# Kernel tuning notes

Hardware: AMD Instinct MI355X
Metric: run time of the kernel (lower is better)

## Reference

```python
import jax, jax.numpy as jnp
import numpy as np

NU = 200000  # num_users
NI = 200000  # num_items
D = 128      # d_model
B = 4096     # interaction batch


def setup_inputs() -> dict:
    key = jax.random.key(0)
    ks = jax.random.split(key, 24)
    f = lambda k, s, sc=1.0: (jax.random.normal(k, s, dtype=jnp.float32) * sc)
    s = 1.0 / np.sqrt(D)
    return {
        "user_id": jax.random.randint(ks[0], (B,), 0, NU),
        "prev_item_id": jax.random.randint(ks[1], (B,), 0, NI),
        "item_id": jax.random.randint(ks[2], (B,), 0, NI),
        "time_since_prev_item": jax.random.uniform(ks[3], (B, 1), dtype=jnp.float32),
        "time_since_prev_user": jax.random.uniform(ks[4], (B, 1), dtype=jnp.float32),
        "dynamic_user_emb": f(ks[5], (NU, D), 0.1),
        "dynamic_item_emb": f(ks[6], (NI, D), 0.1),
        "is_user_new": jnp.ones((NU, 1), dtype=jnp.float32),
        "is_item_new": jnp.ones((NI, 1), dtype=jnp.float32),
        "static_user_W": f(ks[7], (NU, D)),
        "static_item_W": f(ks[8], (NI, D)),
        "initial_user_emb": f(ks[9], (1, D)),
        "initial_item_emb": f(ks[10], (1, D)),
        "user_Wih": f(ks[11], (D, D + 1), s),
        "user_Whh": f(ks[12], (D, D), s),
        "user_bih": f(ks[13], (D,), s),
        "user_bhh": f(ks[14], (D,), s),
        "item_Wih": f(ks[15], (D, D + 1), s),
        "item_Whh": f(ks[16], (D, D), s),
        "item_bih": f(ks[17], (D,), s),
        "item_bhh": f(ks[18], (D,), s),
        "pred_W": f(ks[19], (2 * D, 4 * D), 1.0 / np.sqrt(4 * D)),
        "pred_b": f(ks[20], (2 * D,), 1.0 / np.sqrt(4 * D)),
        "td_W": f(ks[21], (D, 1)),
        "td_b": f(ks[22], (D,)),
    }


def _rnn_cell(x, h, Wih, Whh, bih, bhh):
    # torch.nn.RNNCell: tanh(x @ Wih^T + bih + h @ Whh^T + bhh)
    return jnp.tanh(x @ Wih.T + bih + h @ Whh.T + bhh)


def reference(user_id, prev_item_id, item_id, time_since_prev_item, time_since_prev_user,
              dynamic_user_emb, dynamic_item_emb, is_user_new, is_item_new,
              static_user_W, static_item_W, initial_user_emb, initial_item_emb,
              user_Wih, user_Whh, user_bih, user_bhh,
              item_Wih, item_Whh, item_bih, item_bhh,
              pred_W, pred_b, td_W, td_b):
    # gather dynamic embeddings (fall back to initial emb for new entities)
    user_emb = is_user_new[user_id] * initial_user_emb + dynamic_user_emb[user_id]
    item_emb = is_item_new[item_id] * initial_item_emb + dynamic_item_emb[item_id]
    prev_item_emb = is_item_new[prev_item_id] * initial_item_emb + dynamic_item_emb[prev_item_id]
    static_user_emb = static_user_W[user_id]
    static_item_emb = static_item_W[item_id]
    prev_static_item_emb = static_item_W[prev_item_id]

    # time projection + prediction head
    user_proj = user_emb * (1.0 + time_since_prev_item @ td_W.T + td_b)
    item_pred = jnp.concatenate(
        [user_proj, prev_item_emb, prev_static_item_emb, static_user_emb], axis=1) @ pred_W.T + pred_b
    item_target = jnp.concatenate([item_emb, static_item_emb], axis=1)

    # RNNCell updates
    updated_user_emb = _rnn_cell(jnp.concatenate([item_emb, time_since_prev_item], axis=1),
                                 user_emb, user_Wih, user_Whh, user_bih, user_bhh)
    updated_item_emb = _rnn_cell(jnp.concatenate([user_emb, time_since_prev_user], axis=1),
                                 item_emb, item_Wih, item_Whh, item_bih, item_bhh)

    # scatter back into persistent buffers (detached, as in torch)
    new_dyn_user = dynamic_user_emb.at[user_id].set(jax.lax.stop_gradient(updated_user_emb))
    new_dyn_item = dynamic_item_emb.at[item_id].set(jax.lax.stop_gradient(updated_item_emb))
    new_is_user_new = is_user_new.at[user_id].set(0.0)
    new_is_item_new = is_item_new.at[item_id].set(0.0)

    return (item_pred, item_target, updated_user_emb, user_emb, updated_item_emb, item_emb,
            new_dyn_user, new_dyn_item, new_is_user_new, new_is_item_new)
```

## Files before the change

### kernel.cpp

```cpp
#include <hip/hip_runtime.h>
#include <hip/hip_bf16.h>

#define NU 200000
#define NI 200000
#define D 128
#define BATCH 4096

typedef __bf16 bf16x8 __attribute__((ext_vector_type(8)));
typedef float f32x4 __attribute__((ext_vector_type(4)));

__device__ __forceinline__ void store_bf16x4(__hip_bfloat16* p, float4 v) {
    union { __hip_bfloat16 h[4]; uint2 u; } pk;
    pk.h[0] = __float2bfloat16(v.x);
    pk.h[1] = __float2bfloat16(v.y);
    pk.h[2] = __float2bfloat16(v.z);
    pk.h[3] = __float2bfloat16(v.w);
    *reinterpret_cast<uint2*>(p) = pk.u;
}

__device__ __forceinline__ float4 f4_fma(float s, float4 a, float4 b) {
    return make_float4(fmaf(s, a.x, b.x), fmaf(s, a.y, b.y),
                       fmaf(s, a.z, b.z), fmaf(s, a.w, b.w));
}

__global__ __launch_bounds__(256) void prep_kernel(
    const float* __restrict__ predW,
    const float* __restrict__ uWih, const float* __restrict__ uWhh,
    const float* __restrict__ iWih, const float* __restrict__ iWhh,
    const float* __restrict__ ubih, const float* __restrict__ ubhh,
    const float* __restrict__ ibih, const float* __restrict__ ibhh,
    const int* __restrict__ uid, const int* __restrict__ iid,
    __hip_bfloat16* __restrict__ wPred,
    __hip_bfloat16* __restrict__ wU, __hip_bfloat16* __restrict__ wI,
    float* __restrict__ biasU, float* __restrict__ biasI,
    int* __restrict__ lastU, int* __restrict__ lastI)
{
    int idx = blockIdx.x * 256 + threadIdx.x;
    if (idx < 131072) {
        wPred[idx] = __float2bfloat16(predW[idx]);
        return;
    }
    idx -= 131072;
    if (idx < 73728) {
        int z = idx / 36864;
        int r = idx - z * 36864;
        int j = r / 288, k = r - (r / 288) * 288;
        const float* Wih = z ? iWih : uWih;
        const float* Whh = z ? iWhh : uWhh;
        float v = 0.0f;
        if (k < 128)      v = Whh[j * 128 + k];
        else if (k < 257) v = Wih[j * 129 + (k - 128)];
        __hip_bfloat16* W = z ? wI : wU;
        W[j * 288 + k] = __float2bfloat16(v);
        return;
    }
    idx -= 73728;
    if (idx < 128) { biasU[idx] = ubih[idx] + ubhh[idx]; return; }
    idx -= 128;
    if (idx < 128) { biasI[idx] = ibih[idx] + ibhh[idx]; return; }
    idx -= 128;
    if (idx < BATCH) { atomicMax(&lastU[uid[idx]], idx); return; }
    idx -= BATCH;
    if (idx < BATCH) { atomicMax(&lastI[iid[idx]], idx); return; }
}

__global__ __launch_bounds__(256) void gather_copy_kernel(
    const int* __restrict__ uid, const int* __restrict__ pid,
    const int* __restrict__ iid,
    const float* __restrict__ t_i, const float* __restrict__ t_u,
    const float* __restrict__ dynU, const float* __restrict__ dynI,
    const float* __restrict__ isU, const float* __restrict__ isI,
    const float* __restrict__ statU, const float* __restrict__ statI,
    const float* __restrict__ initU, const float* __restrict__ initI,
    const float* __restrict__ tdW, const float* __restrict__ tdb,
    float* __restrict__ o_user_emb, float* __restrict__ o_item_emb,
    float* __restrict__ o_target,
    __hip_bfloat16* __restrict__ xpred,
    __hip_bfloat16* __restrict__ xhU, __hip_bfloat16* __restrict__ xhI,
    float4* __restrict__ oDynU, float4* __restrict__ oDynI,
    float4* __restrict__ oIsU, float4* __restrict__ oIsI)
{
    long long idx = (long long)blockIdx.x * 256 + threadIdx.x;
    if (idx < 131072) {
        int b = (int)(idx >> 5);
        int g = (int)(idx & 31);
        const float4* dU4 = (const float4*)dynU;
        const float4* dI4 = (const float4*)dynI;
        const float4* sU4 = (const float4*)statU;
        const float4* sI4 = (const float4*)statI;

        int u = uid[b], i = iid[b], p = pid[b];
        float fu = isU[u], fi = isI[i], fp = isI[p];
        float ti = t_i[b], tu = t_u[b];

        float4 iu = ((const float4*)initU)[g];
        float4 ii = ((const float4*)initI)[g];
        float4 ue = f4_fma(fu, iu, dU4[(size_t)u * 32 + g]);
        float4 ie = f4_fma(fi, ii, dI4[(size_t)i * 32 + g]);
        float4 pe = f4_fma(fp, ii, dI4[(size_t)p * 32 + g]);
        float4 su = sU4[(size_t)u * 32 + g];
        float4 si = sI4[(size_t)i * 32 + g];
        float4 sp = sI4[(size_t)p * 32 + g];
        float4 tw = ((const float4*)tdW)[g];
        float4 tb = ((const float4*)tdb)[g];

        ((float4*)o_user_emb)[(size_t)b * 32 + g] = ue;
        ((float4*)o_item_emb)[(size_t)b * 32 + g] = ie;
        ((float4*)o_target)[(size_t)b * 64 + g] = ie;
        ((float4*)o_target)[(size_t)b * 64 + 32 + g] = si;

        float4 f = f4_fma(ti, tw, tb);
        float4 proj = make_float4(ue.x * (1.0f + f.x), ue.y * (1.0f + f.y),
                                  ue.z * (1.0f + f.z), ue.w * (1.0f + f.w));

        __hip_bfloat16* xp = xpred + (size_t)b * 512;
        store_bf16x4(xp + 4 * g, proj);
        store_bf16x4(xp + 128 + 4 * g, pe);
        store_bf16x4(xp + 256 + 4 * g, sp);
        store_bf16x4(xp + 384 + 4 * g, su);

        __hip_bfloat16* xu = xhU + (size_t)b * 288;
        store_bf16x4(xu + 4 * g, ue);
        store_bf16x4(xu + 128 + 4 * g, ie);
        __hip_bfloat16* xi = xhI + (size_t)b * 288;
        store_bf16x4(xi + 4 * g, ie);
        store_bf16x4(xi + 128 + 4 * g, ue);
        if (g < 8) {
            float4 zu = make_float4(g == 0 ? ti : 0.0f, 0.0f, 0.0f, 0.0f);
            float4 zi = make_float4(g == 0 ? tu : 0.0f, 0.0f, 0.0f, 0.0f);
            store_bf16x4(xu + 256 + 4 * g, zu);
            store_bf16x4(xi + 256 + 4 * g, zi);
        }
        return;
    }
    idx -= 131072;
    if (idx < 6400000) { oDynU[idx] = ((const float4*)dynU)[idx]; return; }
    idx -= 6400000;
    if (idx < 6400000) { oDynI[idx] = ((const float4*)dynI)[idx]; return; }
    idx -= 6400000;
    if (idx < 50000) { oIsU[idx] = ((const float4*)isU)[idx]; return; }
    idx -= 50000;
    if (idx < 50000) { oIsI[idx] = ((const float4*)isI)[idx]; return; }
}

__global__ __launch_bounds__(256) void gemm_fused(
    const __hip_bfloat16* __restrict__ xpred,
    const __hip_bfloat16* __restrict__ wPred,
    const float* __restrict__ predb, float* __restrict__ o_pred,
    const __hip_bfloat16* __restrict__ xhU, const __hip_bfloat16* __restrict__ xhI,
    const __hip_bfloat16* __restrict__ wU, const __hip_bfloat16* __restrict__ wI,
    const float* __restrict__ biasU, const float* __restrict__ biasI,
    const int* __restrict__ uid, const int* __restrict__ iid,
    const int* __restrict__ lastU, const int* __restrict__ lastI,
    float* __restrict__ o_updU, float* __restrict__ o_updI,
    float* __restrict__ o_dynU, float* __restrict__ o_dynI,
    float* __restrict__ o_isU, float* __restrict__ o_isI)
{
    int bx = blockIdx.x;
    int tid = threadIdx.x;
    int wave = tid >> 6, lane = tid & 63, quad = lane >> 4, l15 = lane & 15;

    if (bx < 256) {
        const int K = 512;
        int m0 = (bx & 63) * 64, n0 = (bx >> 6) * 64;
        f32x4 acc[4] = {};
        const __hip_bfloat16* Arow = xpred + (size_t)(m0 + wave * 16 + l15) * K;
        for (int k0 = 0; k0 < K; k0 += 32) {
            bf16x8 a = *reinterpret_cast<const bf16x8*>(Arow + k0 + quad * 8);
#pragma unroll
            for (int ct = 0; ct < 4; ++ct) {
                bf16x8 b = *reinterpret_cast<const bf16x8*>(
                    wPred + (size_t)(n0 + ct * 16 + l15) * K + k0 + quad * 8);
                acc[ct] = __builtin_amdgcn_mfma_f32_16x16x32_bf16(a, b, acc[ct], 0, 0, 0);
            }
        }
        int orow = m0 + wave * 16 + quad * 4;
#pragma unroll
        for (int ct = 0; ct < 4; ++ct) {
            int col = n0 + ct * 16 + l15;
            float bc = predb[col];
#pragma unroll
            for (int r = 0; r < 4; ++r)
                o_pred[(size_t)(orow + r) * 256 + col] = acc[ct][r] + bc;
        }
    } else {
        bx -= 256;
        int z = bx >> 7; bx &= 127;
        int m0 = (bx & 63) * 64, n0 = (bx >> 6) * 64;
        const __hip_bfloat16* A = z ? xhI : xhU;
        const __hip_bfloat16* W = z ? wI : wU;
        const float* bias = z ? biasI : biasU;
        const int* ids  = z ? iid : uid;
        const int* last = z ? lastI : lastU;
        float* outB = z ? o_updI : o_updU;
        float* outD = z ? o_dynI : o_dynU;
        float* oIs  = z ? o_isI  : o_isU;

        const int K = 288;
        f32x4 acc[4] = {};
        const __hip_bfloat16* Arow = A + (size_t)(m0 + wave * 16 + l15) * K;
        for (int k0 = 0; k0 < K; k0 += 32) {
            bf16x8 a = *reinterpret_cast<const bf16x8*>(Arow + k0 + quad * 8);
#pragma unroll
            for (int ct = 0; ct < 4; ++ct) {
                bf16x8 b = *reinterpret_cast<const bf16x8*>(
                    W + (size_t)(n0 + ct * 16 + l15) * K + k0 + quad * 8);
                acc[ct] = __builtin_amdgcn_mfma_f32_16x16x32_bf16(a, b, acc[ct], 0, 0, 0);
            }
        }
        int orow = m0 + wave * 16 + quad * 4;
        int rid[4], win[4];
#pragma unroll
        for (int r = 0; r < 4; ++r) {
            int row = orow + r;
            rid[r] = ids[row];
            win[r] = (last[rid[r]] == row);
        }
#pragma unroll
        for (int ct = 0; ct < 4; ++ct) {
            int col = n0 + ct * 16 + l15;
            float bc = bias[col];
#pragma unroll
            for (int r = 0; r < 4; ++r) {
                float v = tanhf(acc[ct][r] + bc);
                outB[(size_t)(orow + r) * D + col] = v;
                if (win[r]) outD[(size_t)rid[r] * D + col] = v;
            }
        }
        if (n0 == 0 && l15 == 0) {
#pragma unroll
            for (int r = 0; r < 4; ++r) oIs[rid[r]] = 0.0f;
        }
    }
}

extern "C" void kernel_launch(void* const* d_in, const int* in_sizes, int n_in,
                              void* d_out, int out_size, void* d_ws, size_t ws_size,
                              hipStream_t stream) {
    const int*   uid   = (const int*)d_in[0];
    const int*   pid   = (const int*)d_in[1];
    const int*   iid   = (const int*)d_in[2];
    const float* t_i   = (const float*)d_in[3];
    const float* t_u   = (const float*)d_in[4];
    const float* dynU  = (const float*)d_in[5];
    const float* dynI  = (const float*)d_in[6];
    const float* isU   = (const float*)d_in[7];
    const float* isI   = (const float*)d_in[8];
    const float* statU = (const float*)d_in[9];
    const float* statI = (const float*)d_in[10];
    const float* initU = (const float*)d_in[11];
    const float* initI = (const float*)d_in[12];
    const float* uWih  = (const float*)d_in[13];
    const float* uWhh  = (const float*)d_in[14];
    const float* ubih  = (const float*)d_in[15];
    const float* ubhh  = (const float*)d_in[16];
    const float* iWih  = (const float*)d_in[17];
    const float* iWhh  = (const float*)d_in[18];
    const float* ibih  = (const float*)d_in[19];
    const float* ibhh  = (const float*)d_in[20];
    const float* predW = (const float*)d_in[21];
    const float* predb = (const float*)d_in[22];
    const float* tdW   = (const float*)d_in[23];
    const float* tdb   = (const float*)d_in[24];

    float* out = (float*)d_out;
    float* o_pred     = out;
    float* o_target   = out + 1048576;
    float* o_updU     = out + 2097152;
    float* o_userEmb  = out + 2621440;
    float* o_updI     = out + 3145728;
    float* o_itemEmb  = out + 3670016;
    float* o_dynU     = out + 4194304;
    float* o_dynI     = out + 29794304;
    float* o_isU      = out + 55394304;
    float* o_isI      = out + 55594304;

    char* ws = (char*)d_ws;
    int* lastU = (int*)ws;
    int* lastI = lastU + NU;
    __hip_bfloat16* xpred = (__hip_bfloat16*)(ws + 1600000);
    __hip_bfloat16* xhU   = (__hip_bfloat16*)(ws + 5794304);
    __hip_bfloat16* xhI   = (__hip_bfloat16*)(ws + 8153600);
    __hip_bfloat16* wPred = (__hip_bfloat16*)(ws + 10512896);
    __hip_bfloat16* wU    = (__hip_bfloat16*)(ws + 10775040);
    __hip_bfloat16* wI    = (__hip_bfloat16*)(ws + 10848768);
    float* biasU = (float*)(ws + 10922496);
    float* biasI = (float*)(ws + 10923008);

    hipMemsetAsync(lastU, 0xFF, (size_t)(NU + NI) * sizeof(int), stream);

    prep_kernel<<<833, 256, 0, stream>>>(
        predW, uWih, uWhh, iWih, iWhh, ubih, ubhh, ibih, ibhh,
        uid, iid, wPred, wU, wI, biasU, biasI, lastU, lastI);

    gather_copy_kernel<<<50903, 256, 0, stream>>>(
        uid, pid, iid, t_i, t_u, dynU, dynI, isU, isI, statU, statI,
        initU, initI, tdW, tdb, o_userEmb, o_itemEmb, o_target,
        xpred, xhU, xhI,
        (float4*)o_dynU, (float4*)o_dynI, (float4*)o_isU, (float4*)o_isI);

    gemm_fused<<<512, 256, 0, stream>>>(
        xpred, wPred, predb, o_pred,
        xhU, xhI, wU, wI, biasU, biasI,
        uid, iid, lastU, lastI,
        o_updU, o_updI, o_dynU, o_dynI, o_isU, o_isI);
}
```

Before: 497.5 us.

## Merge gather into prep and overlap masked table copy with GEMM kernel

The gather step is folded into the prep kernel, and the large dynamic-embedding table copy moves into the GEMM kernel as extra blocks. Those copy blocks skip rows that the GEMM scatter will overwrite, which makes the copy and the scatter disjoint and removes the write-after-write ordering issue. The copy now uses nontemporal loads and stores, and the is_new flags are computed by masking with the last-writer index rather than a separate scatter. This drops one launch and lets the GEMM overlap the bandwidth-bound copy. The cost is a per-thread read of the last-index table and divergent copy blocks.

```diff
diff --git a/kernel.cpp b/kernel.cpp
--- a/kernel.cpp
+++ b/kernel.cpp
@@ -23,19 +23,83 @@
                        fmaf(s, a.z, b.z), fmaf(s, a.w, b.w));
 }
 
-__global__ __launch_bounds__(256) void prep_kernel(
+__global__ __launch_bounds__(256) void prep_gather_kernel(
+    const int* __restrict__ uid, const int* __restrict__ pid,
+    const int* __restrict__ iid,
+    const float* __restrict__ t_i, const float* __restrict__ t_u,
+    const float* __restrict__ dynU, const float* __restrict__ dynI,
+    const float* __restrict__ isU, const float* __restrict__ isI,
+    const float* __restrict__ statU, const float* __restrict__ statI,
+    const float* __restrict__ initU, const float* __restrict__ initI,
+    const float* __restrict__ tdW, const float* __restrict__ tdb,
     const float* __restrict__ predW,
     const float* __restrict__ uWih, const float* __restrict__ uWhh,
     const float* __restrict__ iWih, const float* __restrict__ iWhh,
     const float* __restrict__ ubih, const float* __restrict__ ubhh,
     const float* __restrict__ ibih, const float* __restrict__ ibhh,
-    const int* __restrict__ uid, const int* __restrict__ iid,
+    float* __restrict__ o_user_emb, float* __restrict__ o_item_emb,
+    float* __restrict__ o_target,
+    __hip_bfloat16* __restrict__ xpred,
+    __hip_bfloat16* __restrict__ xhU, __hip_bfloat16* __restrict__ xhI,
     __hip_bfloat16* __restrict__ wPred,
     __hip_bfloat16* __restrict__ wU, __hip_bfloat16* __restrict__ wI,
     float* __restrict__ biasU, float* __restrict__ biasI,
     int* __restrict__ lastU, int* __restrict__ lastI)
 {
     int idx = blockIdx.x * 256 + threadIdx.x;
+    if (idx < 131072) {
+        int b = idx >> 5;
+        int g = idx & 31;
+        const float4* dU4 = (const float4*)dynU;
+        const float4* dI4 = (const float4*)dynI;
+        const float4* sU4 = (const float4*)statU;
+        const float4* sI4 = (const float4*)statI;
+
+        int u = uid[b], i = iid[b], p = pid[b];
+        float fu = isU[u], fi = isI[i], fp = isI[p];
+        float ti = t_i[b], tu = t_u[b];
+
+        float4 iu = ((const float4*)initU)[g];
+        float4 ii = ((const float4*)initI)[g];
+        float4 ue = f4_fma(fu, iu, dU4[(size_t)u * 32 + g]);
+        float4 ie = f4_fma(fi, ii, dI4[(size_t)i * 32 + g]);
+        float4 pe = f4_fma(fp, ii, dI4[(size_t)p * 32 + g]);
+        float4 su = sU4[(size_t)u * 32 + g];
+        float4 si = sI4[(size_t)i * 32 + g];
+        float4 sp = sI4[(size_t)p * 32 + g];
+        float4 tw = ((const float4*)tdW)[g];
+        float4 tb = ((const float4*)tdb)[g];
+
+        ((float4*)o_user_emb)[(size_t)b * 32 + g] = ue;
+        ((float4*)o_item_emb)[(size_t)b * 32 + g] = ie;
+        ((float4*)o_target)[(size_t)b * 64 + g] = ie;
+        ((float4*)o_target)[(size_t)b * 64 + 32 + g] = si;
+
+        float4 f = f4_fma(ti, tw, tb);
+        float4 proj = make_float4(ue.x * (1.0f + f.x), ue.y * (1.0f + f.y),
+                                  ue.z * (1.0f + f.z), ue.w * (1.0f + f.w));
+
+        __hip_bfloat16* xp = xpred + (size_t)b * 512;
+        store_bf16x4(xp + 4 * g, proj);
+        store_bf16x4(xp + 128 + 4 * g, pe);
+        store_bf16x4(xp + 256 + 4 * g, sp);
+        store_bf16x4(xp + 384 + 4 * g, su);
+
+        __hip_bfloat16* xu = xhU + (size_t)b * 288;
+        store_bf16x4(xu + 4 * g, ue);
+        store_bf16x4(xu + 128 + 4 * g, ie);
+        __hip_bfloat16* xi = xhI + (size_t)b * 288;
+        store_bf16x4(xi + 4 * g, ie);
+        store_bf16x4(xi + 128 + 4 * g, ue);
+        if (g < 8) {
+            float4 zu = make_float4(g == 0 ? ti : 0.0f, 0.0f, 0.0f, 0.0f);
+            float4 zi = make_float4(g == 0 ? tu : 0.0f, 0.0f, 0.0f, 0.0f);
+            store_bf16x4(xu + 256 + 4 * g, zu);
+            store_bf16x4(xi + 256 + 4 * g, zi);
+        }
+        return;
+    }
+    idx -= 131072;
     if (idx < 131072) {
         wPred[idx] = __float2bfloat16(predW[idx]);
         return;
@@ -64,86 +128,7 @@
     if (idx < BATCH) { atomicMax(&lastI[iid[idx]], idx); return; }
 }
 
-__global__ __launch_bounds__(256) void gather_copy_kernel(
-    const int* __restrict__ uid, const int* __restrict__ pid,
-    const int* __restrict__ iid,
-    const float* __restrict__ t_i, const float* __restrict__ t_u,
-    const float* __restrict__ dynU, const float* __restrict__ dynI,
-    const float* __restrict__ isU, const float* __restrict__ isI,
-    const float* __restrict__ statU, const float* __restrict__ statI,
-    const float* __restrict__ initU, const float* __restrict__ initI,
-    const float* __restrict__ tdW, const float* __restrict__ tdb,
-    float* __restrict__ o_user_emb, float* __restrict__ o_item_emb,
-    float* __restrict__ o_target,
-    __hip_bfloat16* __restrict__ xpred,
-    __hip_bfloat16* __restrict__ xhU, __hip_bfloat16* __restrict__ xhI,
-    float4* __restrict__ oDynU, float4* __restrict__ oDynI,
-    float4* __restrict__ oIsU, float4* __restrict__ oIsI)
-{
-    long long idx = (long long)blockIdx.x * 256 + threadIdx.x;
-    if (idx < 131072) {
-        int b = (int)(idx >> 5);
-        int g = (int)(idx & 31);
-        const float4* dU4 = (const float4*)dynU;
-        const float4* dI4 = (const float4*)dynI;
-        const float4* sU4 = (const float4*)statU;
-        const float4* sI4 = (const float4*)statI;
-
-        int u = uid[b], i = iid[b], p = pid[b];
-        float fu = isU[u], fi = isI[i], fp = isI[p];
-        float ti = t_i[b], tu = t_u[b];
-
-        float4 iu = ((const float4*)initU)[g];
-        float4 ii = ((const float4*)initI)[g];
-        float4 ue = f4_fma(fu, iu, dU4[(size_t)u * 32 + g]);
-        float4 ie = f4_fma(fi, ii, dI4[(size_t)i * 32 + g]);
-        float4 pe = f4_fma(fp, ii, dI4[(size_t)p * 32 + g]);
-        float4 su = sU4[(size_t)u * 32 + g];
-        float4 si = sI4[(size_t)i * 32 + g];
-        float4 sp = sI4[(size_t)p * 32 + g];
-        float4 tw = ((const float4*)tdW)[g];
-        float4 tb = ((const float4*)tdb)[g];
-
-        ((float4*)o_user_emb)[(size_t)b * 32 + g] = ue;
-        ((float4*)o_item_emb)[(size_t)b * 32 + g] = ie;
-        ((float4*)o_target)[(size_t)b * 64 + g] = ie;
-        ((float4*)o_target)[(size_t)b * 64 + 32 + g] = si;
-
-        float4 f = f4_fma(ti, tw, tb);
-        float4 proj = make_float4(ue.x * (1.0f + f.x), ue.y * (1.0f + f.y),
-                                  ue.z * (1.0f + f.z), ue.w * (1.0f + f.w));
-
-        __hip_bfloat16* xp = xpred + (size_t)b * 512;
-        store_bf16x4(xp + 4 * g, proj);
-        store_bf16x4(xp + 128 + 4 * g, pe);
-        store_bf16x4(xp + 256 + 4 * g, sp);
-        store_bf16x4(xp + 384 + 4 * g, su);
-
-        __hip_bfloat16* xu = xhU + (size_t)b * 288;
-        store_bf16x4(xu + 4 * g, ue);
-        store_bf16x4(xu + 128 + 4 * g, ie);
-        __hip_bfloat16* xi = xhI + (size_t)b * 288;
-        store_bf16x4(xi + 4 * g, ie);
-        store_bf16x4(xi + 128 + 4 * g, ue);
-        if (g < 8) {
-            float4 zu = make_float4(g == 0 ? ti : 0.0f, 0.0f, 0.0f, 0.0f);
-            float4 zi = make_float4(g == 0 ? tu : 0.0f, 0.0f, 0.0f, 0.0f);
-            store_bf16x4(xu + 256 + 4 * g, zu);
-            store_bf16x4(xi + 256 + 4 * g, zi);
-        }
-        return;
-    }
-    idx -= 131072;
-    if (idx < 6400000) { oDynU[idx] = ((const float4*)dynU)[idx]; return; }
-    idx -= 6400000;
-    if (idx < 6400000) { oDynI[idx] = ((const float4*)dynI)[idx]; return; }
-    idx -= 6400000;
-    if (idx < 50000) { oIsU[idx] = ((const float4*)isU)[idx]; return; }
-    idx -= 50000;
-    if (idx < 50000) { oIsI[idx] = ((const float4*)isI)[idx]; return; }
-}
-
-__global__ __launch_bounds__(256) void gemm_fused(
+__global__ __launch_bounds__(256) void gemm_copy_kernel(
     const __hip_bfloat16* __restrict__ xpred,
     const __hip_bfloat16* __restrict__ wPred,
     const float* __restrict__ predb, float* __restrict__ o_pred,
@@ -154,10 +139,57 @@
     const int* __restrict__ lastU, const int* __restrict__ lastI,
     float* __restrict__ o_updU, float* __restrict__ o_updI,
     float* __restrict__ o_dynU, float* __restrict__ o_dynI,
+    const float* __restrict__ dynU, const float* __restrict__ dynI,
+    const float* __restrict__ isU, const float* __restrict__ isI,
     float* __restrict__ o_isU, float* __restrict__ o_isI)
 {
     int bx = blockIdx.x;
     int tid = threadIdx.x;
+
+    if (bx >= 512) {
+        int idx = (bx - 512) * 256 + tid;
+        if (idx < 6400000) {
+            int row = idx >> 5;
+            if (lastU[row] < 0) {
+                f32x4 v = __builtin_nontemporal_load((const f32x4*)dynU + idx);
+                __builtin_nontemporal_store(v, (f32x4*)o_dynU + idx);
+            }
+            return;
+        }
+        idx -= 6400000;
+        if (idx < 6400000) {
+            int row = idx >> 5;
+            if (lastI[row] < 0) {
+                f32x4 v = __builtin_nontemporal_load((const f32x4*)dynI + idx);
+                __builtin_nontemporal_store(v, (f32x4*)o_dynI + idx);
+            }
+            return;
+        }
+        idx -= 6400000;
+        if (idx < 50000) {
+            int4 l = ((const int4*)lastU)[idx];
+            float4 v = ((const float4*)isU)[idx];
+            float4 o = make_float4(l.x >= 0 ? 0.0f : v.x,
+                                   l.y >= 0 ? 0.0f : v.y,
+                                   l.z >= 0 ? 0.0f : v.z,
+                                   l.w >= 0 ? 0.0f : v.w);
+            ((float4*)o_isU)[idx] = o;
+            return;
+        }
+        idx -= 50000;
+        if (idx < 50000) {
+            int4 l = ((const int4*)lastI)[idx];
+            float4 v = ((const float4*)isI)[idx];
+            float4 o = make_float4(l.x >= 0 ? 0.0f : v.x,
+                                   l.y >= 0 ? 0.0f : v.y,
+                                   l.z >= 0 ? 0.0f : v.z,
+                                   l.w >= 0 ? 0.0f : v.w);
+            ((float4*)o_isI)[idx] = o;
+            return;
+        }
+        return;
+    }
+
     int wave = tid >> 6, lane = tid & 63, quad = lane >> 4, l15 = lane & 15;
 
     if (bx < 256) {
@@ -194,7 +226,6 @@
         const int* last = z ? lastI : lastU;
         float* outB = z ? o_updI : o_updU;
         float* outD = z ? o_dynI : o_dynU;
-        float* oIs  = z ? o_isI  : o_isU;
 
         const int K = 288;
         f32x4 acc[4] = {};
@@ -226,10 +257,6 @@
                 outB[(size_t)(orow + r) * D + col] = v;
                 if (win[r]) outD[(size_t)rid[r] * D + col] = v;
             }
-        }
-        if (n0 == 0 && l15 == 0) {
-#pragma unroll
-            for (int r = 0; r < 4; ++r) oIs[rid[r]] = 0.0f;
         }
     }
 }
@@ -289,19 +316,17 @@
 
     hipMemsetAsync(lastU, 0xFF, (size_t)(NU + NI) * sizeof(int), stream);
 
-    prep_kernel<<<833, 256, 0, stream>>>(
+    prep_gather_kernel<<<1345, 256, 0, stream>>>(
+        uid, pid, iid, t_i, t_u, dynU, dynI, isU, isI, statU, statI,
+        initU, initI, tdW, tdb,
         predW, uWih, uWhh, iWih, iWhh, ubih, ubhh, ibih, ibhh,
-        uid, iid, wPred, wU, wI, biasU, biasI, lastU, lastI);
-
-    gather_copy_kernel<<<50903, 256, 0, stream>>>(
-        uid, pid, iid, t_i, t_u, dynU, dynI, isU, isI, statU, statI,
-        initU, initI, tdW, tdb, o_userEmb, o_itemEmb, o_target,
-        xpred, xhU, xhI,
-        (float4*)o_dynU, (float4*)o_dynI, (float4*)o_isU, (float4*)o_isI);
-
-    gemm_fused<<<512, 256, 0, stream>>>(
+        o_userEmb, o_itemEmb, o_target, xpred, xhU, xhI,
+        wPred, wU, wI, biasU, biasI, lastU, lastI);
+
+    gemm_copy_kernel<<<50903, 256, 0, stream>>>(
         xpred, wPred, predb, o_pred,
         xhU, xhI, wU, wI, biasU, biasI,
         uid, iid, lastU, lastI,
-        o_updU, o_updI, o_dynU, o_dynI, o_isU, o_isI);
-}
+        o_updU, o_updI, o_dynU, o_dynI,
+        dynU, dynI, isU, isI, o_isU, o_isI);
+}
```

Result: no change. 505.0 us (+1.5%).
